# Optimization experiments

Measured on AMD Instinct MI355X. Metric: run time of the kernel, lower is better.

## Reference

```python
import jax, jax.numpy as jnp
import numpy as np

B, D, E, H, C = 2048, 1024, 8, 4096, 1024
TOP_K = 2
LN_EPS = 1e-5


def setup_inputs() -> dict:
    key = jax.random.key(0)
    ks = jax.random.split(key, 5)
    x = jax.random.normal(ks[0], (B, D), dtype=jnp.float32)
    Wr = jax.random.normal(ks[1], (D, E), dtype=jnp.float32) * 0.02
    br = jnp.zeros((E,), dtype=jnp.float32)
    ln_g = jnp.ones((E, D), dtype=jnp.float32)
    ln_b = jnp.zeros((E, D), dtype=jnp.float32)
    W1 = jax.random.normal(ks[2], (E, D, H), dtype=jnp.float32) * 0.02
    b1 = jnp.zeros((E, H), dtype=jnp.float32)
    W2 = jax.random.normal(ks[3], (E, H, C), dtype=jnp.float32) * 0.02
    b2 = jnp.zeros((E, C), dtype=jnp.float32)
    return {"x": x, "Wr": Wr, "br": br, "ln_g": ln_g, "ln_b": ln_b,
            "W1": W1, "b1": b1, "W2": W2, "b2": b2}


def reference(x, Wr, br, ln_g, ln_b, W1, b1, W2, b2):
    # Router (eval mode: no jitter)
    router_logits = x @ Wr + br                       # [B, E]
    topk_vals, topk_idx = jax.lax.top_k(router_logits, TOP_K)
    topk_w = jax.nn.softmax(topk_vals, axis=-1)       # [B, K]
    # Scatter top-k weights into a dense [B, E] combine matrix (indices unique per row)
    w_full = jnp.zeros((x.shape[0], E), dtype=x.dtype)
    w_full = w_full.at[jnp.arange(x.shape[0])[:, None], topk_idx].set(topk_w)
    # Shared LayerNorm statistics, per-expert affine
    mu = jnp.mean(x, axis=-1, keepdims=True)
    var = jnp.mean(jnp.square(x - mu), axis=-1, keepdims=True)
    xn = (x - mu) * jax.lax.rsqrt(var + LN_EPS)       # [B, D]
    xe = xn[:, None, :] * ln_g[None] + ln_b[None]     # [B, E, D]
    # Expert MLPs (dense over experts; combine weights zero-out non-selected experts)
    h = jax.nn.gelu(jnp.einsum('bed,edh->beh', xe, W1) + b1[None], approximate=False)
    y = jnp.einsum('beh,ehc->bec', h, W2) + b2[None]  # [B, E, C]
    out = jnp.einsum('be,bec->bc', w_full, y)         # weighted combine
    return out
```

## Files before the change

kernel.cpp:

```cpp
#include <hip/hip_runtime.h>
#include <hip/hip_bf16.h>

#define B_TOK 2048
#define D_DIM 1024
#define E_NUM 8
#define H_DIM 4096
#define C_DIM 1024
#define CAP   5120
#define MAXT  40

typedef __attribute__((ext_vector_type(8))) short bf16x8;
typedef __attribute__((ext_vector_type(4))) float floatx4;

__device__ __forceinline__ unsigned short f2bf(float f) {
  union { float f; unsigned int u; } a; a.f = f;
  unsigned int u = a.u;
  return (unsigned short)((u + 0x7FFFu + ((u >> 16) & 1u)) >> 16);
}

__device__ __forceinline__ void gload_lds16(const void* g, void* l) {
  __builtin_amdgcn_global_load_lds(
      (const __attribute__((address_space(1))) void*)g,
      (__attribute__((address_space(3))) void*)l, 16, 0, 0);
}

__global__ __launch_bounds__(256) void kinit(float* out_acc, int* slot_tok, int* counts) {
  int id = blockIdx.x * 256 + threadIdx.x;
  out_acc[id] = 0.f;
  if (id < CAP) slot_tok[id] = -1;
  if (id < E_NUM) counts[id] = 0;
}

__global__ __launch_bounds__(256) void krouter(const float* __restrict__ x,
                                               const float* __restrict__ Wr,
                                               const float* __restrict__ br,
                                               int2* meta_i, float4* meta_f, int* counts) {
  int b = blockIdx.x, t = threadIdx.x;
  const float4 xv = *(const float4*)(x + (size_t)b * D_DIM + t * 4);
  float v[10];
  v[0] = xv.x + xv.y + xv.z + xv.w;
  v[1] = xv.x * xv.x + xv.y * xv.y + xv.z * xv.z + xv.w * xv.w;
#pragma unroll
  for (int e = 0; e < 8; e++) v[2 + e] = 0.f;
  const float* wr = Wr + (size_t)(t * 4) * E_NUM;
  float xs[4] = {xv.x, xv.y, xv.z, xv.w};
#pragma unroll
  for (int j = 0; j < 4; j++) {
    float4 wa = *(const float4*)(wr + j * 8);
    float4 wb = *(const float4*)(wr + j * 8 + 4);
    v[2] += xs[j] * wa.x; v[3] += xs[j] * wa.y; v[4] += xs[j] * wa.z; v[5] += xs[j] * wa.w;
    v[6] += xs[j] * wb.x; v[7] += xs[j] * wb.y; v[8] += xs[j] * wb.z; v[9] += xs[j] * wb.w;
  }
#pragma unroll
  for (int i = 0; i < 10; i++) {
    float s = v[i];
#pragma unroll
    for (int off = 32; off > 0; off >>= 1) s += __shfl_down(s, off, 64);
    v[i] = s;
  }
  __shared__ float red[4][10];
  int lane = t & 63, wid = t >> 6;
  if (lane == 0) {
#pragma unroll
    for (int i = 0; i < 10; i++) red[wid][i] = v[i];
  }
  __syncthreads();
  if (t == 0) {
    float f[10];
#pragma unroll
    for (int i = 0; i < 10; i++) f[i] = red[0][i] + red[1][i] + red[2][i] + red[3][i];
    float mu = f[0] * (1.f / 1024.f);
    float var = f[1] * (1.f / 1024.f) - mu * mu;
    float rsig = rsqrtf(var + 1e-5f);
    float lg[8];
#pragma unroll
    for (int e = 0; e < 8; e++) lg[e] = f[2 + e] + br[e];
    int i0 = 0;
#pragma unroll
    for (int e = 1; e < 8; e++) if (lg[e] > lg[i0]) i0 = e;
    int i1 = (i0 == 0) ? 1 : 0;
#pragma unroll
    for (int e = 0; e < 8; e++) if (e != i0 && lg[e] > lg[i1]) i1 = e;
    float ex = expf(lg[i1] - lg[i0]);
    float w0 = 1.f / (1.f + ex);
    float w1 = 1.f - w0;
    atomicAdd(counts + i0, 1);
    atomicAdd(counts + i1, 1);
    meta_i[b] = make_int2(i0, i1);
    meta_f[b] = make_float4(w0, w1, mu, rsig);
  }
}

__global__ void kprefix(const int* counts, int* cursor, int* tmap_e, int* tmap_r) {
  if (threadIdx.x == 0) {
    int total = 0, tt = 0;
    for (int e = 0; e < E_NUM; e++) {
      cursor[e] = total;
      int nt = (counts[e] + 127) >> 7;
      for (int i = 0; i < nt; i++) { tmap_e[tt] = e; tmap_r[tt] = total + i * 128; tt++; }
      total += nt << 7;
    }
    for (; tt < MAXT; tt++) tmap_e[tt] = -1;
  }
}

__global__ __launch_bounds__(256) void kscatter(const float* __restrict__ x,
                                                const float* __restrict__ ln_g,
                                                const float* __restrict__ ln_b,
                                                const int2* __restrict__ meta_i,
                                                const float4* __restrict__ meta_f,
                                                int* cursor, int* slot_tok, float* slot_w,
                                                unsigned short* __restrict__ xe) {
  int b = blockIdx.x, t = threadIdx.x;
  __shared__ int se[2], ss[2];
  __shared__ float smu, srs;
  if (t == 0) {
    int2 mi = meta_i[b];
    float4 mf = meta_f[b];
    int s0 = atomicAdd(cursor + mi.x, 1);
    int s1 = atomicAdd(cursor + mi.y, 1);
    slot_tok[s0] = b; slot_w[s0] = mf.x;
    slot_tok[s1] = b; slot_w[s1] = mf.y;
    se[0] = mi.x; se[1] = mi.y; ss[0] = s0; ss[1] = s1;
    smu = mf.z; srs = mf.w;
  }
  __syncthreads();
  int i = t * 4;
  float4 xv = *(const float4*)(x + (size_t)b * D_DIM + i);
  float mu = smu, rs = srs;
  float xn0 = (xv.x - mu) * rs, xn1 = (xv.y - mu) * rs, xn2 = (xv.z - mu) * rs, xn3 = (xv.w - mu) * rs;
#pragma unroll
  for (int k = 0; k < 2; k++) {
    int e = se[k], s = ss[k];
    float4 g = *(const float4*)(ln_g + (size_t)e * D_DIM + i);
    float4 bb = *(const float4*)(ln_b + (size_t)e * D_DIM + i);
    union { unsigned short us[4]; uint2 v; } u;
    u.us[0] = f2bf(xn0 * g.x + bb.x);
    u.us[1] = f2bf(xn1 * g.y + bb.y);
    u.us[2] = f2bf(xn2 * g.z + bb.z);
    u.us[3] = f2bf(xn3 * g.w + bb.w);
    *(uint2*)(xe + (size_t)s * D_DIM + i) = u.v;
  }
}

__global__ __launch_bounds__(256) void ktranspose(const float* __restrict__ src,
                                                  unsigned short* __restrict__ dst,
                                                  int R, int C) {
  __shared__ float tile[64][65];
  int z = blockIdx.z;
  const float* s = src + (size_t)z * R * C;
  unsigned short* d = dst + (size_t)z * R * C;
  int cx = blockIdx.x * 64, ry = blockIdx.y * 64;
  int t = threadIdx.x;
  int cl4 = (t & 15) * 4, rl = t >> 4;
#pragma unroll
  for (int p = 0; p < 4; p++) {
    int r = rl + p * 16;
    float4 v = *(const float4*)(s + (size_t)(ry + r) * C + cx + cl4);
    tile[r][cl4] = v.x; tile[r][cl4 + 1] = v.y; tile[r][cl4 + 2] = v.z; tile[r][cl4 + 3] = v.w;
  }
  __syncthreads();
#pragma unroll
  for (int p = 0; p < 4; p++) {
    int c = rl + p * 16;
    union { unsigned short us[4]; uint2 v; } u;
    u.us[0] = f2bf(tile[cl4][c]);
    u.us[1] = f2bf(tile[cl4 + 1][c]);
    u.us[2] = f2bf(tile[cl4 + 2][c]);
    u.us[3] = f2bf(tile[cl4 + 3][c]);
    *(uint2*)(d + (size_t)(cx + c) * R + ry + cl4) = u.v;
  }
}

__global__ __launch_bounds__(256) void kgemm1(const unsigned short* __restrict__ xe,
                                              const unsigned short* __restrict__ w1t,
                                              const float* __restrict__ b1,
                                              unsigned short* __restrict__ h,
                                              const int* __restrict__ tmap_e,
                                              const int* __restrict__ tmap_r) {
  int e = tmap_e[blockIdx.y];
  if (e < 0) return;
  int row0 = tmap_r[blockIdx.y];
  int n0 = blockIdx.x * 128;
  const unsigned short* Ab = xe + (size_t)row0 * D_DIM;
  const unsigned short* Bb = w1t + (size_t)e * H_DIM * D_DIM + (size_t)n0 * D_DIM;
  __shared__ unsigned short As[128 * 32];
  __shared__ unsigned short Bs[128 * 32];
  int t = threadIdx.x, lane = t & 63, wid = t >> 6;
  int c0 = wid * 2, c1 = c0 + 1;
  int lr0 = c0 * 16 + (lane >> 2);
  int kc = (lane & 3) * 8;
  const unsigned short* ga0 = Ab + (size_t)lr0 * D_DIM + kc;
  const unsigned short* ga1 = ga0 + 16 * D_DIM;
  const unsigned short* gb0 = Bb + (size_t)lr0 * D_DIM + kc;
  const unsigned short* gb1 = gb0 + 16 * D_DIM;
  unsigned short* la0 = As + c0 * 512;
  unsigned short* la1 = As + c1 * 512;
  unsigned short* lb0 = Bs + c0 * 512;
  unsigned short* lb1 = Bs + c1 * 512;
  int l15 = lane & 15, q = lane >> 4;
  int wm = (wid & 1) * 64, wn = (wid >> 1) * 64;
  const unsigned short* pa[4];
  const unsigned short* pb[4];
#pragma unroll
  for (int i = 0; i < 4; i++) {
    pa[i] = As + (wm + i * 16 + l15) * 32 + q * 8;
    pb[i] = Bs + (wn + i * 16 + l15) * 32 + q * 8;
  }
  floatx4 acc[4][4];
#pragma unroll
  for (int i = 0; i < 4; i++)
#pragma unroll
    for (int j = 0; j < 4; j++) acc[i][j] = (floatx4){0.f, 0.f, 0.f, 0.f};

  for (int k0 = 0; k0 < D_DIM; k0 += 32) {
    gload_lds16(ga0, la0);
    gload_lds16(ga1, la1);
    gload_lds16(gb0, lb0);
    gload_lds16(gb1, lb1);
    __syncthreads();
    bf16x8 af[4], bfr[4];
#pragma unroll
    for (int i = 0; i < 4; i++) { af[i] = *(const bf16x8*)pa[i]; bfr[i] = *(const bf16x8*)pb[i]; }
#pragma unroll
    for (int mt = 0; mt < 4; mt++)
#pragma unroll
      for (int nt = 0; nt < 4; nt++)
        acc[mt][nt] = __builtin_amdgcn_mfma_f32_16x16x32_bf16(af[mt], bfr[nt], acc[mt][nt], 0, 0, 0);
    __syncthreads();
    ga0 += 32; ga1 += 32; gb0 += 32; gb1 += 32;
  }
  float b1v[4];
#pragma unroll
  for (int nt = 0; nt < 4; nt++) b1v[nt] = b1[(size_t)e * H_DIM + n0 + wn + nt * 16 + l15];
#pragma unroll
  for (int mt = 0; mt < 4; mt++) {
    int row = row0 + wm + mt * 16 + q * 4;
#pragma unroll
    for (int nt = 0; nt < 4; nt++) {
      int col = n0 + wn + nt * 16 + l15;
      unsigned short* hp = h + (size_t)row * H_DIM + col;
#pragma unroll
      for (int r = 0; r < 4; r++) {
        float v = acc[mt][nt][r] + b1v[nt];
        v = 0.5f * v * (1.f + erff(v * 0.70710678118f));
        hp[(size_t)r * H_DIM] = f2bf(v);
      }
    }
  }
}

__global__ __launch_bounds__(256) void kgemm2(const unsigned short* __restrict__ h,
                                              const unsigned short* __restrict__ w2t,
                                              const int* __restrict__ slot_tok,
                                              const float* __restrict__ slot_w,
                                              float* __restrict__ out_acc,
                                              const int* __restrict__ tmap_e,
                                              const int* __restrict__ tmap_r) {
  int e = tmap_e[blockIdx.y];
  if (e < 0) return;
  int row0 = tmap_r[blockIdx.y];
  int n0 = blockIdx.x * 128;
  int kz = blockIdx.z;
  const unsigned short* Ab = h + (size_t)row0 * H_DIM + kz * 2048;
  const unsigned short* Bb = w2t + (size_t)e * C_DIM * H_DIM + (size_t)n0 * H_DIM + kz * 2048;
  __shared__ unsigned short As[128 * 32];
  __shared__ unsigned short Bs[128 * 32];
  __shared__ int stok[128];
  __shared__ float swgt[128];
  int t = threadIdx.x, lane = t & 63, wid = t >> 6;
  if (t < 128) { stok[t] = slot_tok[row0 + t]; swgt[t] = slot_w[row0 + t]; }
  int c0 = wid * 2, c1 = c0 + 1;
  int lr0 = c0 * 16 + (lane >> 2);
  int kc = (lane & 3) * 8;
  const unsigned short* ga0 = Ab + (size_t)lr0 * H_DIM + kc;
  const unsigned short* ga1 = ga0 + (size_t)16 * H_DIM;
  const unsigned short* gb0 = Bb + (size_t)lr0 * H_DIM + kc;
  const unsigned short* gb1 = gb0 + (size_t)16 * H_DIM;
  unsigned short* la0 = As + c0 * 512;
  unsigned short* la1 = As + c1 * 512;
  unsigned short* lb0 = Bs + c0 * 512;
  unsigned short* lb1 = Bs + c1 * 512;
  int l15 = lane & 15, q = lane >> 4;
  int wm = (wid & 1) * 64, wn = (wid >> 1) * 64;
  const unsigned short* pa[4];
  const unsigned short* pb[4];
#pragma unroll
  for (int i = 0; i < 4; i++) {
    pa[i] = As + (wm + i * 16 + l15) * 32 + q * 8;
    pb[i] = Bs + (wn + i * 16 + l15) * 32 + q * 8;
  }
  floatx4 acc[4][4];
#pragma unroll
  for (int i = 0; i < 4; i++)
#pragma unroll
    for (int j = 0; j < 4; j++) acc[i][j] = (floatx4){0.f, 0.f, 0.f, 0.f};

  for (int k0 = 0; k0 < 2048; k0 += 32) {
    gload_lds16(ga0, la0);
    gload_lds16(ga1, la1);
    gload_lds16(gb0, lb0);
    gload_lds16(gb1, lb1);
    __syncthreads();
    bf16x8 af[4], bfr[4];
#pragma unroll
    for (int i = 0; i < 4; i++) { af[i] = *(const bf16x8*)pa[i]; bfr[i] = *(const bf16x8*)pb[i]; }
#pragma unroll
    for (int mt = 0; mt < 4; mt++)
#pragma unroll
      for (int nt = 0; nt < 4; nt++)
        acc[mt][nt] = __builtin_amdgcn_mfma_f32_16x16x32_bf16(af[mt], bfr[nt], acc[mt][nt], 0, 0, 0);
    __syncthreads();
    ga0 += 32; ga1 += 32; gb0 += 32; gb1 += 32;
  }
#pragma unroll
  for (int mt = 0; mt < 4; mt++) {
    int rbase = wm + mt * 16 + q * 4;
#pragma unroll
    for (int nt = 0; nt < 4; nt++) {
      int col = n0 + wn + nt * 16 + l15;
#pragma unroll
      for (int r = 0; r < 4; r++) {
        int tk = stok[rbase + r];
        if (tk >= 0)
          atomicAdd(out_acc + (size_t)tk * C_DIM + col, swgt[rbase + r] * acc[mt][nt][r]);
      }
    }
  }
}

__global__ __launch_bounds__(256) void kfinal(const float* __restrict__ out_acc,
                                              const int2* __restrict__ meta_i,
                                              const float4* __restrict__ meta_f,
                                              const float* __restrict__ b2,
                                              float* __restrict__ out) {
  int b = blockIdx.x, t = threadIdx.x;
  int i = t * 4;
  int2 mi = meta_i[b];
  float4 mf = meta_f[b];
  float4 a = *(const float4*)(out_acc + (size_t)b * C_DIM + i);
  float4 p = *(const float4*)(b2 + (size_t)mi.x * C_DIM + i);
  float4 qv = *(const float4*)(b2 + (size_t)mi.y * C_DIM + i);
  float4 o;
  o.x = a.x + mf.x * p.x + mf.y * qv.x;
  o.y = a.y + mf.x * p.y + mf.y * qv.y;
  o.z = a.z + mf.x * p.z + mf.y * qv.z;
  o.w = a.w + mf.x * p.w + mf.y * qv.w;
  *(float4*)(out + (size_t)b * C_DIM + i) = o;
}

extern "C" void kernel_launch(void* const* d_in, const int* in_sizes, int n_in,
                              void* d_out, int out_size, void* d_ws, size_t ws_size,
                              hipStream_t stream) {
  const float* x    = (const float*)d_in[0];
  const float* Wr   = (const float*)d_in[1];
  const float* br   = (const float*)d_in[2];
  const float* ln_g = (const float*)d_in[3];
  const float* ln_b = (const float*)d_in[4];
  const float* W1   = (const float*)d_in[5];
  const float* b1   = (const float*)d_in[6];
  const float* W2   = (const float*)d_in[7];
  const float* b2   = (const float*)d_in[8];

  char* w = (char*)d_ws;
  auto alloc = [&](size_t sz) { char* p = w; w += (sz + 255) & ~(size_t)255; return p; };
  unsigned short* W1t = (unsigned short*)alloc((size_t)E_NUM * H_DIM * D_DIM * 2);
  unsigned short* W2t = (unsigned short*)alloc((size_t)E_NUM * C_DIM * H_DIM * 2);
  unsigned short* xe  = (unsigned short*)alloc((size_t)CAP * D_DIM * 2);
  unsigned short* hb  = (unsigned short*)alloc((size_t)CAP * H_DIM * 2);
  float* out_acc      = (float*)alloc((size_t)B_TOK * C_DIM * 4);
  int2* meta_i        = (int2*)alloc((size_t)B_TOK * 8);
  float4* meta_f      = (float4*)alloc((size_t)B_TOK * 16);
  int* counts         = (int*)alloc(64);
  int* cursor         = (int*)alloc(64);
  int* tmap_e         = (int*)alloc(MAXT * 4);
  int* tmap_r         = (int*)alloc(MAXT * 4);
  int* slot_tok       = (int*)alloc(CAP * 4);
  float* slot_w       = (float*)alloc(CAP * 4);

  hipLaunchKernelGGL(ktranspose, dim3(H_DIM / 64, D_DIM / 64, E_NUM), dim3(256), 0, stream,
                     W1, W1t, D_DIM, H_DIM);
  hipLaunchKernelGGL(ktranspose, dim3(C_DIM / 64, H_DIM / 64, E_NUM), dim3(256), 0, stream,
                     W2, W2t, H_DIM, C_DIM);
  hipLaunchKernelGGL(kinit, dim3(B_TOK * C_DIM / 256), dim3(256), 0, stream,
                     out_acc, slot_tok, counts);
  hipLaunchKernelGGL(krouter, dim3(B_TOK), dim3(256), 0, stream,
                     x, Wr, br, meta_i, meta_f, counts);
  hipLaunchKernelGGL(kprefix, dim3(1), dim3(64), 0, stream,
                     counts, cursor, tmap_e, tmap_r);
  hipLaunchKernelGGL(kscatter, dim3(B_TOK), dim3(256), 0, stream,
                     x, ln_g, ln_b, meta_i, meta_f, cursor, slot_tok, slot_w, xe);
  hipLaunchKernelGGL(kgemm1, dim3(H_DIM / 128, MAXT), dim3(256), 0, stream,
                     xe, W1t, b1, hb, tmap_e, tmap_r);
  hipLaunchKernelGGL(kgemm2, dim3(C_DIM / 128, MAXT, 2), dim3(256), 0, stream,
                     hb, W2t, slot_tok, slot_w, out_acc, tmap_e, tmap_r);
  hipLaunchKernelGGL(kfinal, dim3(B_TOK), dim3(256), 0, stream,
                     out_acc, meta_i, meta_f, b2, (float*)d_out);
}
```

Before: 577.9 us.

## Replace atomic scatter-add combine with split-K partial buffers gathered in final kernel

The second GEMM now writes its two split-K partial results as plain stores into a per-slot buffer instead of doing weighted float atomics into a per-token accumulator. The final kernel gathers both partials for each of the token's two slots and applies the routing weights and bias there. This drops the output zero-init pass, the slot token and weight arrays, and the atomic contention. In exchange it writes and reads a larger partial buffer (2×CAP×C floats).

New measurement: 584.4 us. Within noise of the previous version (+1.1%).

```diff
diff --git a/kernel.cpp b/kernel.cpp
--- a/kernel.cpp
+++ b/kernel.cpp
@@ -24,11 +24,8 @@
       (__attribute__((address_space(3))) void*)l, 16, 0, 0);
 }
 
-__global__ __launch_bounds__(256) void kinit(float* out_acc, int* slot_tok, int* counts) {
-  int id = blockIdx.x * 256 + threadIdx.x;
-  out_acc[id] = 0.f;
-  if (id < CAP) slot_tok[id] = -1;
-  if (id < E_NUM) counts[id] = 0;
+__global__ void kinit(int* counts) {
+  if (threadIdx.x < E_NUM) counts[threadIdx.x] = 0;
 }
 
 __global__ __launch_bounds__(256) void krouter(const float* __restrict__ x,
@@ -109,7 +106,7 @@
                                                 const float* __restrict__ ln_b,
                                                 const int2* __restrict__ meta_i,
                                                 const float4* __restrict__ meta_f,
-                                                int* cursor, int* slot_tok, float* slot_w,
+                                                int* cursor, int2* meta_s,
                                                 unsigned short* __restrict__ xe) {
   int b = blockIdx.x, t = threadIdx.x;
   __shared__ int se[2], ss[2];
@@ -119,8 +116,7 @@
     float4 mf = meta_f[b];
     int s0 = atomicAdd(cursor + mi.x, 1);
     int s1 = atomicAdd(cursor + mi.y, 1);
-    slot_tok[s0] = b; slot_w[s0] = mf.x;
-    slot_tok[s1] = b; slot_w[s1] = mf.y;
+    meta_s[b] = make_int2(s0, s1);
     se[0] = mi.x; se[1] = mi.y; ss[0] = s0; ss[1] = s1;
     smu = mf.z; srs = mf.w;
   }
@@ -252,9 +248,7 @@
 
 __global__ __launch_bounds__(256) void kgemm2(const unsigned short* __restrict__ h,
                                               const unsigned short* __restrict__ w2t,
-                                              const int* __restrict__ slot_tok,
-                                              const float* __restrict__ slot_w,
-                                              float* __restrict__ out_acc,
+                                              float* __restrict__ ypart,
                                               const int* __restrict__ tmap_e,
                                               const int* __restrict__ tmap_r) {
   int e = tmap_e[blockIdx.y];
@@ -264,12 +258,10 @@
   int kz = blockIdx.z;
   const unsigned short* Ab = h + (size_t)row0 * H_DIM + kz * 2048;
   const unsigned short* Bb = w2t + (size_t)e * C_DIM * H_DIM + (size_t)n0 * H_DIM + kz * 2048;
+  float* yo = ypart + (size_t)kz * CAP * C_DIM;
   __shared__ unsigned short As[128 * 32];
   __shared__ unsigned short Bs[128 * 32];
-  __shared__ int stok[128];
-  __shared__ float swgt[128];
   int t = threadIdx.x, lane = t & 63, wid = t >> 6;
-  if (t < 128) { stok[t] = slot_tok[row0 + t]; swgt[t] = slot_w[row0 + t]; }
   int c0 = wid * 2, c1 = c0 + 1;
   int lr0 = c0 * 16 + (lane >> 2);
   int kc = (lane & 3) * 8;
@@ -315,37 +307,41 @@
   }
 #pragma unroll
   for (int mt = 0; mt < 4; mt++) {
-    int rbase = wm + mt * 16 + q * 4;
+    int rbase = row0 + wm + mt * 16 + q * 4;
 #pragma unroll
     for (int nt = 0; nt < 4; nt++) {
       int col = n0 + wn + nt * 16 + l15;
 #pragma unroll
-      for (int r = 0; r < 4; r++) {
-        int tk = stok[rbase + r];
-        if (tk >= 0)
-          atomicAdd(out_acc + (size_t)tk * C_DIM + col, swgt[rbase + r] * acc[mt][nt][r]);
-      }
+      for (int r = 0; r < 4; r++)
+        yo[(size_t)(rbase + r) * C_DIM + col] = acc[mt][nt][r];
     }
   }
 }
 
-__global__ __launch_bounds__(256) void kfinal(const float* __restrict__ out_acc,
+__global__ __launch_bounds__(256) void kfinal(const float* __restrict__ ypart,
                                               const int2* __restrict__ meta_i,
+                                              const int2* __restrict__ meta_s,
                                               const float4* __restrict__ meta_f,
                                               const float* __restrict__ b2,
                                               float* __restrict__ out) {
   int b = blockIdx.x, t = threadIdx.x;
   int i = t * 4;
   int2 mi = meta_i[b];
+  int2 ms = meta_s[b];
   float4 mf = meta_f[b];
-  float4 a = *(const float4*)(out_acc + (size_t)b * C_DIM + i);
+  const float* y0 = ypart;
+  const float* y1 = ypart + (size_t)CAP * C_DIM;
+  float4 a0 = *(const float4*)(y0 + (size_t)ms.x * C_DIM + i);
+  float4 a1 = *(const float4*)(y1 + (size_t)ms.x * C_DIM + i);
+  float4 c0 = *(const float4*)(y0 + (size_t)ms.y * C_DIM + i);
+  float4 c1 = *(const float4*)(y1 + (size_t)ms.y * C_DIM + i);
   float4 p = *(const float4*)(b2 + (size_t)mi.x * C_DIM + i);
   float4 qv = *(const float4*)(b2 + (size_t)mi.y * C_DIM + i);
   float4 o;
-  o.x = a.x + mf.x * p.x + mf.y * qv.x;
-  o.y = a.y + mf.x * p.y + mf.y * qv.y;
-  o.z = a.z + mf.x * p.z + mf.y * qv.z;
-  o.w = a.w + mf.x * p.w + mf.y * qv.w;
+  o.x = mf.x * (a0.x + a1.x + p.x) + mf.y * (c0.x + c1.x + qv.x);
+  o.y = mf.x * (a0.y + a1.y + p.y) + mf.y * (c0.y + c1.y + qv.y);
+  o.z = mf.x * (a0.z + a1.z + p.z) + mf.y * (c0.z + c1.z + qv.z);
+  o.w = mf.x * (a0.w + a1.w + p.w) + mf.y * (c0.w + c1.w + qv.w);
   *(float4*)(out + (size_t)b * C_DIM + i) = o;
 }
 
@@ -368,32 +364,30 @@
   unsigned short* W2t = (unsigned short*)alloc((size_t)E_NUM * C_DIM * H_DIM * 2);
   unsigned short* xe  = (unsigned short*)alloc((size_t)CAP * D_DIM * 2);
   unsigned short* hb  = (unsigned short*)alloc((size_t)CAP * H_DIM * 2);
-  float* out_acc      = (float*)alloc((size_t)B_TOK * C_DIM * 4);
+  float* ypart        = (float*)alloc((size_t)2 * CAP * C_DIM * 4);
   int2* meta_i        = (int2*)alloc((size_t)B_TOK * 8);
+  int2* meta_s        = (int2*)alloc((size_t)B_TOK * 8);
   float4* meta_f      = (float4*)alloc((size_t)B_TOK * 16);
   int* counts         = (int*)alloc(64);
   int* cursor         = (int*)alloc(64);
   int* tmap_e         = (int*)alloc(MAXT * 4);
   int* tmap_r         = (int*)alloc(MAXT * 4);
-  int* slot_tok       = (int*)alloc(CAP * 4);
-  float* slot_w       = (float*)alloc(CAP * 4);
 
   hipLaunchKernelGGL(ktranspose, dim3(H_DIM / 64, D_DIM / 64, E_NUM), dim3(256), 0, stream,
                      W1, W1t, D_DIM, H_DIM);
   hipLaunchKernelGGL(ktranspose, dim3(C_DIM / 64, H_DIM / 64, E_NUM), dim3(256), 0, stream,
                      W2, W2t, H_DIM, C_DIM);
-  hipLaunchKernelGGL(kinit, dim3(B_TOK * C_DIM / 256), dim3(256), 0, stream,
-                     out_acc, slot_tok, counts);
+  hipLaunchKernelGGL(kinit, dim3(1), dim3(64), 0, stream, counts);
   hipLaunchKernelGGL(krouter, dim3(B_TOK), dim3(256), 0, stream,
                      x, Wr, br, meta_i, meta_f, counts);
   hipLaunchKernelGGL(kprefix, dim3(1), dim3(64), 0, stream,
                      counts, cursor, tmap_e, tmap_r);
   hipLaunchKernelGGL(kscatter, dim3(B_TOK), dim3(256), 0, stream,
-                     x, ln_g, ln_b, meta_i, meta_f, cursor, slot_tok, slot_w, xe);
+                     x, ln_g, ln_b, meta_i, meta_f, cursor, meta_s, xe);
   hipLaunchKernelGGL(kgemm1, dim3(H_DIM / 128, MAXT), dim3(256), 0, stream,
                      xe, W1t, b1, hb, tmap_e, tmap_r);
   hipLaunchKernelGGL(kgemm2, dim3(C_DIM / 128, MAXT, 2), dim3(256), 0, stream,
-                     hb, W2t, slot_tok, slot_w, out_acc, tmap_e, tmap_r);
+                     hb, W2t, ypart, tmap_e, tmap_r);
   hipLaunchKernelGGL(kfinal, dim3(B_TOK), dim3(256), 0, stream,
-                     out_acc, meta_i, meta_f, b2, (float*)d_out);
-}
+                     ypart, meta_i, meta_s, meta_f, b2, (float*)d_out);
+}
```
